# Performance work log

Measured on AMD Instinct MI355X. Metric: run time of the kernel, lower is better.

Reference implementation:

```python
import jax, jax.numpy as jnp
import numpy as np
import math

B, N, D, H = 2, 64, 256, 8
DK = D // H


def setup_inputs() -> dict:
    key = jax.random.key(0)
    ks = jax.random.split(key, 12)
    s = 1.0 / math.sqrt(D)
    inp = {
        "state": jax.random.normal(ks[0], (B, N, N, D), dtype=jnp.float32),
        "mask": jnp.zeros((B, N, N, N), dtype=bool),
        "W_lk": jax.random.normal(ks[1], (D, D), dtype=jnp.float32) * s,
        "b_lk": jnp.zeros((D,), dtype=jnp.float32),
        "W_rk": jax.random.normal(ks[2], (D, D), dtype=jnp.float32) * s,
        "b_rk": jnp.zeros((D,), dtype=jnp.float32),
        "W_lv": jax.random.normal(ks[3], (D, D), dtype=jnp.float32) * s,
        "b_lv": jnp.zeros((D,), dtype=jnp.float32),
        "W_rv": jax.random.normal(ks[4], (D, D), dtype=jnp.float32) * s,
        "b_rv": jnp.zeros((D,), dtype=jnp.float32),
        "W_o": jax.random.normal(ks[5], (D, D), dtype=jnp.float32) * s,
        "b_o": jnp.zeros((D,), dtype=jnp.float32),
    }
    return inp


def _proj(x, W, b):
    # torch nn.Linear: x @ W.T + b, then view to heads
    y = jnp.einsum('bxyd,ed->bxye', x, W) + b
    return y.reshape(B, N, N, H, DK)


def reference(state, mask, W_lk, b_lk, W_rk, b_rk, W_lv, b_lv, W_rv, b_rv, W_o, b_o):
    left_k = _proj(state, W_lk, b_lk)   # [B,N,N,H,DK]
    right_k = _proj(state, W_rk, b_rk)
    left_v = _proj(state, W_lv, b_lv)
    right_v = _proj(state, W_rv, b_rv)

    # triangle-style scores over node triples (x, a, y): [B,N,N,N,H]
    scores = jnp.einsum('bxahd,bayhd->bxayh', left_k, right_k) / math.sqrt(DK)
    scores = jnp.where(mask[..., None], jnp.float32(-1000.0), scores)
    att = jax.nn.softmax(scores, axis=2)  # softmax over intermediate node a

    # val[b,x,a,y,h,d] = left_v[b,x,a,h,d] * right_v[b,a,y,h,d] (materialized as in torch)
    val = jnp.einsum('bxahd,bayhd->bxayhd', left_v, right_v)
    x = jnp.einsum('bxayh,bxayhd->bxyhd', att, val)  # sum over a
    x = x.reshape(B, N, N, D)
    return jnp.einsum('bxyd,ed->bxye', x, W_o) + b_o
```

## Files before the change

### kernel.cpp

```cpp
#include <hip/hip_runtime.h>

#define B 2
#define N 64
#define D 256
#define H 8
#define DK 32
#define M (B * N * N)

typedef __attribute__((ext_vector_type(8))) short bf16x8;
typedef __attribute__((ext_vector_type(4))) float f32x4;
typedef __attribute__((ext_vector_type(2))) float f32x2;

#define PROJ_ELEMS (2097152)

__device__ __forceinline__ ushort f2b(float f) {
    union { float f; unsigned u; } v; v.f = f;
    unsigned r = v.u + 0x7fffu + ((v.u >> 16) & 1u);
    return (ushort)(r >> 16);
}
__device__ __forceinline__ float b2f(ushort u) {
    union { unsigned u; float f; } v; v.u = ((unsigned)u) << 16; return v.f;
}
__device__ __forceinline__ f32x2 up2(unsigned u) {
    union { unsigned u; float f; } lo, hi;
    lo.u = u << 16; hi.u = u & 0xffff0000u;
    f32x2 r; r.x = lo.f; r.y = hi.f; return r;
}

__device__ __forceinline__ void glds16(const ushort* g, ushort* l) {
    __builtin_amdgcn_global_load_lds(
        (const __attribute__((address_space(1))) unsigned int*)g,
        (__attribute__((address_space(3))) unsigned int*)l, 16, 0, 0);
}

__global__ __launch_bounds__(256) void cast_all(const float* __restrict__ state,
                                                const float* __restrict__ W_lk, const float* __restrict__ W_rk,
                                                const float* __restrict__ W_lv, const float* __restrict__ W_rv,
                                                const float* __restrict__ W_o,
                                                const float* __restrict__ b_lk, const float* __restrict__ b_rk,
                                                const float* __restrict__ b_lv, const float* __restrict__ b_rv,
                                                const float* __restrict__ b_o,
                                                ushort* __restrict__ state_bf,
                                                ushort* __restrict__ Wcat,
                                                float* __restrict__ bias_cat) {
    const int gid = blockIdx.x * 256 + threadIdx.x;
    const float* Ws[5] = {W_lk, W_rk, W_lv, W_rv, W_o};
    const float* bs[5] = {b_lk, b_rk, b_lv, b_rv, b_o};

    if (gid < 1280) bias_cat[gid] = bs[gid >> 8][gid & 255];

    if (gid < 524288) {
        float4 v = *(const float4*)&state[(size_t)gid * 4];
        ushort4 o = {f2b(v.x), f2b(v.y), f2b(v.z), f2b(v.w)};
        *(ushort4*)&state_bf[(size_t)gid * 4] = o;
    } else {
        int u = gid - 524288;
        int row = u >> 6;
        int k4 = (u & 63) * 4;
        const float* W = Ws[row >> 8];
        float4 v = *(const float4*)&W[(size_t)(row & 255) * 256 + k4];
        ushort4 o = {f2b(v.x), f2b(v.y), f2b(v.z), f2b(v.w)};
        *(ushort4*)&Wcat[(size_t)row * 256 + k4] = o;
    }
}

template <int BF16OUT, int RELAYOUT>
__global__ __launch_bounds__(256) void gemm_mfma(const ushort* __restrict__ A,
                                                 const ushort* __restrict__ Bw,
                                                 const float* __restrict__ bias,
                                                 void* __restrict__ Cv, int ldc) {
    __shared__ __align__(16) ushort As[4][128 * 32];
    __shared__ __align__(16) ushort Bs[4][128 * 32];
    const int tid = threadIdx.x;
    const int lane = tid & 63;
    const int wave = tid >> 6;
    const int wm = (wave & 1) * 64;
    const int wn = (wave >> 1) * 64;
    const int row0 = blockIdx.x * 128;
    const int col0 = blockIdx.y * 128;

    const int lr = lane >> 2;
    const int lkq = (lane & 3) * 8;

    const ushort* gA0 = A + (size_t)(row0 + wave * 32 + lr) * 256 + lkq;
    const ushort* gA1 = gA0 + 16 * 256;
    const ushort* gB0 = Bw + (size_t)(col0 + wave * 32 + lr) * 256 + lkq;
    const ushort* gB1 = gB0 + 16 * 256;

    const int fr = lane & 15;
    const int fk = (lane >> 4) * 8;

    f32x4 acc[4][4] = {};

    for (int half = 0; half < 2; ++half) {
        const int k0 = half * 128;
        __syncthreads();
#pragma unroll
        for (int pp = 0; pp < 4; ++pp) {
            glds16(gA0 + k0 + pp * 32, &As[pp][(wave * 32) * 32]);
            glds16(gA1 + k0 + pp * 32, &As[pp][(wave * 32 + 16) * 32]);
            glds16(gB0 + k0 + pp * 32, &Bs[pp][(wave * 32) * 32]);
            glds16(gB1 + k0 + pp * 32, &Bs[pp][(wave * 32 + 16) * 32]);
        }
        __syncthreads();

#pragma unroll
        for (int pp = 0; pp < 4; ++pp) {
            bf16x8 af[4], bf[4];
#pragma unroll
            for (int i = 0; i < 4; ++i)
                af[i] = *(const bf16x8*)&As[pp][(wm + i * 16 + fr) * 32 + fk];
#pragma unroll
            for (int j = 0; j < 4; ++j)
                bf[j] = *(const bf16x8*)&Bs[pp][(wn + j * 16 + fr) * 32 + fk];
#pragma unroll
            for (int i = 0; i < 4; ++i)
#pragma unroll
                for (int j = 0; j < 4; ++j)
                    acc[i][j] = __builtin_amdgcn_mfma_f32_16x16x32_bf16(af[i], bf[j], acc[i][j], 0, 0, 0);
        }
    }

#pragma unroll
    for (int j = 0; j < 4; ++j) {
        const int col = col0 + wn + j * 16 + (lane & 15);
        const float bv = bias[col];
#pragma unroll
        for (int i = 0; i < 4; ++i) {
            const int rbase = row0 + wm + i * 16 + (lane >> 4) * 4;
#pragma unroll
            for (int r = 0; r < 4; ++r) {
                float o = acc[i][j][r] + bv;
                if (RELAYOUT) {
                    const int row = rbase + r;
                    const int bb = row >> 12, rr = row & 4095;
                    const int proj = col >> 8, hh = (col >> 5) & 7, dk = col & 31;
                    ((ushort*)Cv)[(size_t)proj * PROJ_ELEMS +
                                  ((size_t)(bb * 8 + hh) * 4096 + rr) * 32 + dk] = f2b(o);
                } else if (BF16OUT) {
                    ((ushort*)Cv)[(size_t)(rbase + r) * ldc + col] = f2b(o);
                } else {
                    ((float*)Cv)[(size_t)(rbase + r) * ldc + col] = o;
                }
            }
        }
    }
}

__global__ __launch_bounds__(512, 2) void fused_attn(const ushort* __restrict__ P,
                                                     const unsigned char* __restrict__ mask,
                                                     ushort* __restrict__ xbuf) {
    __shared__ __align__(16) ushort LVb[2][16 * 512];
    __shared__ __align__(16) ushort RVb[2][16 * 512];
    __shared__ __align__(16) float atts[16 * 16 * 20];
    __shared__ float mstate[16 * 20];
    __shared__ float lstate[16 * 20];
    __shared__ float alphas[16 * 20];

    const int bh = blockIdx.z;
    const int b = bh >> 3, h = bh & 7;
    const int x0 = blockIdx.x * 16, y0 = blockIdx.y * 16;
    const int tid = threadIdx.x;
    const int lane = tid & 63, wave = tid >> 6;

    const size_t HB = (size_t)bh * 4096 * 32;
    const ushort* PLK = P + HB;
    const ushort* PRK = P + (size_t)1 * PROJ_ELEMS + HB;
    const ushort* PLV = P + (size_t)2 * PROJ_ELEMS + HB;
    const ushort* PRV = P + (size_t)3 * PROJ_ELEMS + HB;

    const int gy = lane >> 2;
    const int du = lane & 3;
    const int sx = tid >> 4, sy = tid & 15;
    if (tid < 256) {
        mstate[sx * 20 + sy] = -3.0e38f;
        lstate[sx * 20 + sy] = 0.0f;
    }

    const int sa = lane >> 2, soct = lane & 3;
    const int r2 = wave * 2;

    f32x2 acc[2][4] = {};
    const float scale = 0.17677669529663687f;

#define STAGE(ac_, buf_)                                                                     \
    do {                                                                                     \
        glds16(PLV + ((size_t)(x0 + r2) * 64 + (ac_) + sa) * 32 + soct * 8,                  \
               &LVb[buf_][r2 * 512]);                                                        \
        glds16(PLV + ((size_t)(x0 + r2 + 1) * 64 + (ac_) + sa) * 32 + soct * 8,              \
               &LVb[buf_][(r2 + 1) * 512]);                                                  \
        glds16(PRV + ((size_t)((ac_) + r2) * 64 + y0 + sa) * 32 + soct * 8,                  \
               &RVb[buf_][r2 * 512]);                                                        \
        glds16(PRV + ((size_t)((ac_) + r2 + 1) * 64 + y0 + sa) * 32 + soct * 8,              \
               &RVb[buf_][(r2 + 1) * 512]);                                                  \
    } while (0)

    STAGE(0, 0);

    for (int c = 0; c < 4; ++c) {
        const int ac = c * 16;
        const int cur = c & 1;
        __syncthreads();

        {
            const int fr = lane & 15, fk = (lane >> 4) * 8;
            const int yq = lane & 15, xq = (lane >> 4) * 4;
#pragma unroll
            for (int aw = 0; aw < 2; ++aw) {
                const int a = wave * 2 + aw;
                bf16x8 af = *(const bf16x8*)&PLK[((size_t)(x0 + fr) * 64 + ac + a) * 32 + fk];
                bf16x8 bf = *(const bf16x8*)&PRK[((size_t)(ac + a) * 64 + y0 + fr) * 32 + fk];
                f32x4 s = {};
                s = __builtin_amdgcn_mfma_f32_16x16x32_bf16(af, bf, s, 0, 0, 0);
#pragma unroll
                for (int rr = 0; rr < 4; ++rr) {
                    const int x = xq + rr;
                    float sv = s[rr] * scale;
                    if (mask[((size_t)(b * N + x0 + x) * N + ac + a) * N + y0 + yq]) sv = -1000.0f;
                    atts[(a * 16 + x) * 20 + yq] = sv;
                }
            }
        }
        __syncthreads();

        if (tid < 256) {
            float mc = -3.0e38f;
#pragma unroll
            for (int a = 0; a < 16; ++a) mc = fmaxf(mc, atts[(a * 16 + sx) * 20 + sy]);
            const float mold = mstate[sx * 20 + sy];
            const float mnew = fmaxf(mold, mc);
            const float alpha = __expf(mold - mnew);
            float ps = 0.0f;
#pragma unroll
            for (int a = 0; a < 16; ++a) {
                float p = __expf(atts[(a * 16 + sx) * 20 + sy] - mnew);
                atts[(a * 16 + sx) * 20 + sy] = p;
                ps += p;
            }
            lstate[sx * 20 + sy] = lstate[sx * 20 + sy] * alpha + ps;
            mstate[sx * 20 + sy] = mnew;
            alphas[sx * 20 + sy] = alpha;
        }
        __syncthreads();

        if (c < 3) STAGE(ac + 16, cur ^ 1);

#pragma unroll
        for (int i = 0; i < 2; ++i) {
            const float av = alphas[(wave * 2 + i) * 20 + gy];
#pragma unroll
            for (int q = 0; q < 4; ++q) acc[i][q] *= av;
        }

        {
            const unsigned* LV32 = (const unsigned*)&LVb[cur][0];
            const unsigned* RV32 = (const unsigned*)&RVb[cur][0];
#pragma unroll
            for (int a = 0; a < 16; ++a) {
                const uint4 rvw = *(const uint4*)&RV32[a * 256 + gy * 16 + du * 4];
                const f32x2 rv0 = up2(rvw.x), rv1 = up2(rvw.y);
                const f32x2 rv2 = up2(rvw.z), rv3 = up2(rvw.w);
#pragma unroll
                for (int i = 0; i < 2; ++i) {
                    const int x = wave * 2 + i;
                    const uint4 lvw = *(const uint4*)&LV32[x * 256 + a * 16 + du * 4];
                    const float w = atts[(a * 16 + x) * 20 + gy];
                    acc[i][0] += (up2(lvw.x) * w) * rv0;
                    acc[i][1] += (up2(lvw.y) * w) * rv1;
                    acc[i][2] += (up2(lvw.z) * w) * rv2;
                    acc[i][3] += (up2(lvw.w) * w) * rv3;
                }
            }
        }
    }

#pragma unroll
    for (int i = 0; i < 2; ++i) {
        const int x = wave * 2 + i;
        const float il = 1.0f / lstate[x * 20 + gy];
        ushort o[8] __attribute__((aligned(16)));
#pragma unroll
        for (int q = 0; q < 4; ++q) {
            o[2 * q]     = f2b(acc[i][q].x * il);
            o[2 * q + 1] = f2b(acc[i][q].y * il);
        }
        *(uint4*)&xbuf[(((size_t)b * N + x0 + x) * N + y0 + gy) * D + h * DK + du * 8] =
            *(const uint4*)o;
    }
#undef STAGE
}

extern "C" void kernel_launch(void* const* d_in, const int* in_sizes, int n_in,
                              void* d_out, int out_size, void* d_ws, size_t ws_size,
                              hipStream_t stream) {
    const float* state = (const float*)d_in[0];
    const unsigned char* mask = (const unsigned char*)d_in[1];
    const float* W_lk = (const float*)d_in[2];
    const float* b_lk = (const float*)d_in[3];
    const float* W_rk = (const float*)d_in[4];
    const float* b_rk = (const float*)d_in[5];
    const float* W_lv = (const float*)d_in[6];
    const float* b_lv = (const float*)d_in[7];
    const float* W_rv = (const float*)d_in[8];
    const float* b_rv = (const float*)d_in[9];
    const float* W_o = (const float*)d_in[10];
    const float* b_o = (const float*)d_in[11];
    float* out = (float*)d_out;

    char* ws = (char*)d_ws;
    ushort* P_bf = (ushort*)ws;
    ws += (size_t)4 * PROJ_ELEMS * 2;
    float* bias_cat = (float*)ws;
    ws += 1280 * 4;
    ushort* state_bf = (ushort*)ws;
    ws += (size_t)M * D * 2;
    ushort* Wcat = (ushort*)ws;
    ws += (size_t)1280 * 256 * 2;
    ushort* xbuf_bf = (ushort*)ws;

    cast_all<<<2368, 256, 0, stream>>>(state, W_lk, W_rk, W_lv, W_rv, W_o,
                                       b_lk, b_rk, b_lv, b_rv, b_o,
                                       state_bf, Wcat, bias_cat);
    gemm_mfma<1, 1><<<dim3(M / 128, 8), 256, 0, stream>>>(state_bf, Wcat, bias_cat, P_bf, 1024);
    fused_attn<<<dim3(4, 4, B * H), 512, 0, stream>>>(P_bf, mask, xbuf_bf);
    gemm_mfma<0, 0><<<dim3(M / 128, 2), 256, 0, stream>>>(xbuf_bf, Wcat + 1024 * 256, bias_cat + 1024, out, 256);
}
```

Measured before the change: 122.1 us.

## Fuse softmax exp into PV accumulation and remap blocks across XCDs

The online-softmax pass now computes only the running max and rescale factor. Each thread evaluates exp(score - max) inside the value-accumulation loop and keeps its own row-sum in a register, so the separate exp/sum pass over the attention tile and the lstate array go away. The launch also changes to a 1D grid whose block index is remapped so that all tiles of one (batch, head) fall on the same XCD, aiming for better L2 reuse of the projection data. The cost is redundant exponentials: each score is now exponentiated by every du lane that reads it, four times per score.

```diff
diff --git a/kernel.cpp b/kernel.cpp
--- a/kernel.cpp
+++ b/kernel.cpp
@@ -153,13 +153,16 @@
     __shared__ __align__(16) ushort LVb[2][16 * 512];
     __shared__ __align__(16) ushort RVb[2][16 * 512];
     __shared__ __align__(16) float atts[16 * 16 * 20];
-    __shared__ float mstate[16 * 20];
-    __shared__ float lstate[16 * 20];
-    __shared__ float alphas[16 * 20];
-
-    const int bh = blockIdx.z;
+    __shared__ float mstate[256];
+    __shared__ float alphas[256];
+
+    const int bid = blockIdx.x;
+    const int xcd = bid & 7;
+    const int q = bid >> 3;
+    const int bh = xcd * 2 + (q >> 4);
+    const int t = q & 15;
     const int b = bh >> 3, h = bh & 7;
-    const int x0 = blockIdx.x * 16, y0 = blockIdx.y * 16;
+    const int x0 = (t & 3) * 16, y0 = (t >> 2) * 16;
     const int tid = threadIdx.x;
     const int lane = tid & 63, wave = tid >> 6;
 
@@ -172,15 +175,13 @@
     const int gy = lane >> 2;
     const int du = lane & 3;
     const int sx = tid >> 4, sy = tid & 15;
-    if (tid < 256) {
-        mstate[sx * 20 + sy] = -3.0e38f;
-        lstate[sx * 20 + sy] = 0.0f;
-    }
+    if (tid < 256) mstate[tid] = -3.0e38f;
 
     const int sa = lane >> 2, soct = lane & 3;
     const int r2 = wave * 2;
 
     f32x2 acc[2][4] = {};
+    float lacc[2] = {0.0f, 0.0f};
     const float scale = 0.17677669529663687f;
 
 #define STAGE(ac_, buf_)                                                                     \
@@ -227,29 +228,24 @@
             float mc = -3.0e38f;
 #pragma unroll
             for (int a = 0; a < 16; ++a) mc = fmaxf(mc, atts[(a * 16 + sx) * 20 + sy]);
-            const float mold = mstate[sx * 20 + sy];
+            const float mold = mstate[tid];
             const float mnew = fmaxf(mold, mc);
-            const float alpha = __expf(mold - mnew);
-            float ps = 0.0f;
-#pragma unroll
-            for (int a = 0; a < 16; ++a) {
-                float p = __expf(atts[(a * 16 + sx) * 20 + sy] - mnew);
-                atts[(a * 16 + sx) * 20 + sy] = p;
-                ps += p;
-            }
-            lstate[sx * 20 + sy] = lstate[sx * 20 + sy] * alpha + ps;
-            mstate[sx * 20 + sy] = mnew;
-            alphas[sx * 20 + sy] = alpha;
+            mstate[tid] = mnew;
+            alphas[tid] = __expf(mold - mnew);
         }
         __syncthreads();
 
         if (c < 3) STAGE(ac + 16, cur ^ 1);
 
+        float mn[2];
 #pragma unroll
         for (int i = 0; i < 2; ++i) {
-            const float av = alphas[(wave * 2 + i) * 20 + gy];
-#pragma unroll
-            for (int q = 0; q < 4; ++q) acc[i][q] *= av;
+            const int x = wave * 2 + i;
+            const float av = alphas[x * 16 + gy];
+            mn[i] = mstate[x * 16 + gy];
+            lacc[i] *= av;
+#pragma unroll
+            for (int qq = 0; qq < 4; ++qq) acc[i][qq] *= av;
         }
 
         {
@@ -264,7 +260,9 @@
                 for (int i = 0; i < 2; ++i) {
                     const int x = wave * 2 + i;
                     const uint4 lvw = *(const uint4*)&LV32[x * 256 + a * 16 + du * 4];
-                    const float w = atts[(a * 16 + x) * 20 + gy];
+                    const float sv = atts[(a * 16 + x) * 20 + gy];
+                    const float w = __expf(sv - mn[i]);
+                    lacc[i] += w;
                     acc[i][0] += (up2(lvw.x) * w) * rv0;
                     acc[i][1] += (up2(lvw.y) * w) * rv1;
                     acc[i][2] += (up2(lvw.z) * w) * rv2;
@@ -277,12 +275,12 @@
 #pragma unroll
     for (int i = 0; i < 2; ++i) {
         const int x = wave * 2 + i;
-        const float il = 1.0f / lstate[x * 20 + gy];
+        const float il = 1.0f / lacc[i];
         ushort o[8] __attribute__((aligned(16)));
 #pragma unroll
-        for (int q = 0; q < 4; ++q) {
-            o[2 * q]     = f2b(acc[i][q].x * il);
-            o[2 * q + 1] = f2b(acc[i][q].y * il);
+        for (int qq = 0; qq < 4; ++qq) {
+            o[2 * qq]     = f2b(acc[i][qq].x * il);
+            o[2 * qq + 1] = f2b(acc[i][qq].y * il);
         }
         *(uint4*)&xbuf[(((size_t)b * N + x0 + x) * N + y0 + gy) * D + h * DK + du * 8] =
             *(const uint4*)o;
@@ -322,6 +320,6 @@
                                        b_lk, b_rk, b_lv, b_rv, b_o,
                                        state_bf, Wcat, bias_cat);
     gemm_mfma<1, 1><<<dim3(M / 128, 8), 256, 0, stream>>>(state_bf, Wcat, bias_cat, P_bf, 1024);
-    fused_attn<<<dim3(4, 4, B * H), 512, 0, stream>>>(P_bf, mask, xbuf_bf);
+    fused_attn<<<256, 512, 0, stream>>>(P_bf, mask, xbuf_bf);
     gemm_mfma<0, 0><<<dim3(M / 128, 2), 256, 0, stream>>>(xbuf_bf, Wcat + 1024 * 256, bias_cat + 1024, out, 256);
 }
```

Measured after the change: 126.0 us. 1.03x slower.

## Process 32-wide a-chunks per iteration and drop double-buffered LV/RV staging

Applied to the files above, without the earlier changes.

Replaces the four-chunk double-buffered pipeline (16 intermediate nodes per chunk) with two chunks of 32 nodes, each loaded into single LDS buffers at the start of the iteration. This halves the number of online-softmax rescale steps and barrier rounds per tile. In exchange, loads of the next chunk no longer overlap with the compute of the current one. LDS usage for atts grows, which may affect the two-blocks-per-CU occupancy target. The LDS load completion is presumably covered by the existing barrier after the score computation.

```diff
diff --git a/kernel.cpp b/kernel.cpp
--- a/kernel.cpp
+++ b/kernel.cpp
@@ -150,9 +150,9 @@
 __global__ __launch_bounds__(512, 2) void fused_attn(const ushort* __restrict__ P,
                                                      const unsigned char* __restrict__ mask,
                                                      ushort* __restrict__ xbuf) {
-    __shared__ __align__(16) ushort LVb[2][16 * 512];
-    __shared__ __align__(16) ushort RVb[2][16 * 512];
-    __shared__ __align__(16) float atts[16 * 16 * 20];
+    __shared__ __align__(16) ushort LVb[16 * 1024];
+    __shared__ __align__(16) ushort RVb[32 * 512];
+    __shared__ __align__(16) float atts[32 * 16 * 20];
     __shared__ float mstate[16 * 20];
     __shared__ float lstate[16 * 20];
     __shared__ float alphas[16 * 20];
@@ -179,35 +179,35 @@
 
     const int sa = lane >> 2, soct = lane & 3;
     const int r2 = wave * 2;
+    const int a4 = wave * 4;
 
     f32x2 acc[2][4] = {};
+    float lacc_unused = 0.0f; (void)lacc_unused;
     const float scale = 0.17677669529663687f;
 
-#define STAGE(ac_, buf_)                                                                     \
-    do {                                                                                     \
-        glds16(PLV + ((size_t)(x0 + r2) * 64 + (ac_) + sa) * 32 + soct * 8,                  \
-               &LVb[buf_][r2 * 512]);                                                        \
-        glds16(PLV + ((size_t)(x0 + r2 + 1) * 64 + (ac_) + sa) * 32 + soct * 8,              \
-               &LVb[buf_][(r2 + 1) * 512]);                                                  \
-        glds16(PRV + ((size_t)((ac_) + r2) * 64 + y0 + sa) * 32 + soct * 8,                  \
-               &RVb[buf_][r2 * 512]);                                                        \
-        glds16(PRV + ((size_t)((ac_) + r2 + 1) * 64 + y0 + sa) * 32 + soct * 8,              \
-               &RVb[buf_][(r2 + 1) * 512]);                                                  \
-    } while (0)
-
-    STAGE(0, 0);
-
-    for (int c = 0; c < 4; ++c) {
-        const int ac = c * 16;
-        const int cur = c & 1;
-        __syncthreads();
+    for (int c = 0; c < 2; ++c) {
+        const int ac = c * 32;
+        __syncthreads();
+
+        glds16(PLV + ((size_t)(x0 + r2) * 64 + ac + sa) * 32 + soct * 8,
+               &LVb[r2 * 1024]);
+        glds16(PLV + ((size_t)(x0 + r2) * 64 + ac + 16 + sa) * 32 + soct * 8,
+               &LVb[r2 * 1024 + 512]);
+        glds16(PLV + ((size_t)(x0 + r2 + 1) * 64 + ac + sa) * 32 + soct * 8,
+               &LVb[(r2 + 1) * 1024]);
+        glds16(PLV + ((size_t)(x0 + r2 + 1) * 64 + ac + 16 + sa) * 32 + soct * 8,
+               &LVb[(r2 + 1) * 1024 + 512]);
+#pragma unroll
+        for (int k = 0; k < 4; ++k)
+            glds16(PRV + ((size_t)(ac + a4 + k) * 64 + y0 + sa) * 32 + soct * 8,
+                   &RVb[(a4 + k) * 512]);
 
         {
             const int fr = lane & 15, fk = (lane >> 4) * 8;
             const int yq = lane & 15, xq = (lane >> 4) * 4;
 #pragma unroll
-            for (int aw = 0; aw < 2; ++aw) {
-                const int a = wave * 2 + aw;
+            for (int aw = 0; aw < 4; ++aw) {
+                const int a = wave * 4 + aw;
                 bf16x8 af = *(const bf16x8*)&PLK[((size_t)(x0 + fr) * 64 + ac + a) * 32 + fk];
                 bf16x8 bf = *(const bf16x8*)&PRK[((size_t)(ac + a) * 64 + y0 + fr) * 32 + fk];
                 f32x4 s = {};
@@ -226,13 +226,13 @@
         if (tid < 256) {
             float mc = -3.0e38f;
 #pragma unroll
-            for (int a = 0; a < 16; ++a) mc = fmaxf(mc, atts[(a * 16 + sx) * 20 + sy]);
+            for (int a = 0; a < 32; ++a) mc = fmaxf(mc, atts[(a * 16 + sx) * 20 + sy]);
             const float mold = mstate[sx * 20 + sy];
             const float mnew = fmaxf(mold, mc);
             const float alpha = __expf(mold - mnew);
             float ps = 0.0f;
 #pragma unroll
-            for (int a = 0; a < 16; ++a) {
+            for (int a = 0; a < 32; ++a) {
                 float p = __expf(atts[(a * 16 + sx) * 20 + sy] - mnew);
                 atts[(a * 16 + sx) * 20 + sy] = p;
                 ps += p;
@@ -243,8 +243,6 @@
         }
         __syncthreads();
 
-        if (c < 3) STAGE(ac + 16, cur ^ 1);
-
 #pragma unroll
         for (int i = 0; i < 2; ++i) {
             const float av = alphas[(wave * 2 + i) * 20 + gy];
@@ -253,17 +251,17 @@
         }
 
         {
-            const unsigned* LV32 = (const unsigned*)&LVb[cur][0];
-            const unsigned* RV32 = (const unsigned*)&RVb[cur][0];
-#pragma unroll
-            for (int a = 0; a < 16; ++a) {
+            const unsigned* LV32 = (const unsigned*)LVb;
+            const unsigned* RV32 = (const unsigned*)RVb;
+#pragma unroll
+            for (int a = 0; a < 32; ++a) {
                 const uint4 rvw = *(const uint4*)&RV32[a * 256 + gy * 16 + du * 4];
                 const f32x2 rv0 = up2(rvw.x), rv1 = up2(rvw.y);
                 const f32x2 rv2 = up2(rvw.z), rv3 = up2(rvw.w);
 #pragma unroll
                 for (int i = 0; i < 2; ++i) {
                     const int x = wave * 2 + i;
-                    const uint4 lvw = *(const uint4*)&LV32[x * 256 + a * 16 + du * 4];
+                    const uint4 lvw = *(const uint4*)&LV32[x * 512 + a * 16 + du * 4];
                     const float w = atts[(a * 16 + x) * 20 + gy];
                     acc[i][0] += (up2(lvw.x) * w) * rv0;
                     acc[i][1] += (up2(lvw.y) * w) * rv1;
@@ -287,7 +285,6 @@
         *(uint4*)&xbuf[(((size_t)b * N + x0 + x) * N + y0 + gy) * D + h * DK + du * 8] =
             *(const uint4*)o;
     }
-#undef STAGE
 }
 
 extern "C" void kernel_launch(void* const* d_in, const int* in_sizes, int n_in,
```

Result: no change. 120.9 us (-0.9%).
